# Kernel tuning notes

Measured on AMD Instinct MI355X. Metric: run time of the kernel, lower is better.

The kernel has to match this reference:

```python
import jax, jax.numpy as jnp
import numpy as np

B, L, D, H = 1024, 128, 768, 256
EPS = 1e-5  # torch BatchNorm1d default eps


def _masked_mean(x, lens):
    # x: [B, L, D], lens: [B] int -> mean over first lens[i] rows per sample
    mask = (jnp.arange(x.shape[1])[None, :] < lens[:, None]).astype(x.dtype)  # [B, L]
    return jnp.einsum('bld,bl->bd', x, mask) / lens[:, None].astype(x.dtype)


def _batchnorm_train(x, gamma, beta):
    # training-mode BN: batch mean and biased variance
    mu = jnp.mean(x, axis=0)
    var = jnp.mean((x - mu) ** 2, axis=0)
    return gamma * (x - mu) / jnp.sqrt(var + EPS) + beta


def setup_inputs() -> dict:
    key = jax.random.key(0)
    ks = jax.random.split(key, 12)
    user_features = jax.random.normal(ks[0], (B, L, D), jnp.float32)
    hashtag_features = jax.random.normal(ks[1], (B, L, D), jnp.float32)
    user_lens = jax.random.randint(ks[2], (B,), 1, L + 1, jnp.int32)
    hashtag_lens = jax.random.randint(ks[3], (B,), 1, L + 1, jnp.int32)
    def lin(k, fan_out, fan_in):
        bound = 1.0 / np.sqrt(fan_in)
        kw, kb = jax.random.split(k)
        w = jax.random.uniform(kw, (fan_out, fan_in), jnp.float32, -bound, bound)
        b = jax.random.uniform(kb, (fan_out,), jnp.float32, -bound, bound)
        return w, b
    fc1_w, fc1_b = lin(ks[4], D, 2 * D)
    fc2_w, fc2_b = lin(ks[5], H, D)
    fc3_w, fc3_b = lin(ks[6], 1, H)
    bn1_g = jnp.ones((D,), jnp.float32)
    bn1_b = jnp.zeros((D,), jnp.float32)
    bn2_g = jnp.ones((H,), jnp.float32)
    bn2_b = jnp.zeros((H,), jnp.float32)
    return {
        'user_features': user_features, 'hashtag_features': hashtag_features,
        'user_lens': user_lens, 'hashtag_lens': hashtag_lens,
        'fc1_w': fc1_w, 'fc1_b': fc1_b, 'bn1_g': bn1_g, 'bn1_b': bn1_b,
        'fc2_w': fc2_w, 'fc2_b': fc2_b, 'bn2_g': bn2_g, 'bn2_b': bn2_b,
        'fc3_w': fc3_w, 'fc3_b': fc3_b,
    }


def reference(user_features, hashtag_features, user_lens, hashtag_lens,
              fc1_w, fc1_b, bn1_g, bn1_b, fc2_w, fc2_b, bn2_g, bn2_b,
              fc3_w, fc3_b):
    # fused ragged mean pooling (replaces per-sample python loop)
    u = _masked_mean(user_features, user_lens)       # [B, D]
    h = _masked_mean(hashtag_features, hashtag_lens)  # [B, D]
    x = jnp.concatenate([u, h], axis=1)               # [B, 2D]
    x = jax.nn.relu(_batchnorm_train(x @ fc1_w.T + fc1_b, bn1_g, bn1_b))
    x = jax.nn.relu(_batchnorm_train(x @ fc2_w.T + fc2_b, bn2_g, bn2_b))
    out = jax.nn.sigmoid(x @ fc3_w.T + fc3_b)          # [B, 1]
    return out
```

## Files before the change

kernel.cpp:

```cpp
#include <hip/hip_runtime.h>
#include <cstdint>
#include <cstddef>

#define BATCH 1024
#define SEQL  128
#define DIM   768
#define HID   256
#define KIN1  1536
#define BN_EPS 1e-5f

typedef unsigned short u16;
typedef __attribute__((ext_vector_type(8))) short short8;
typedef __attribute__((ext_vector_type(4))) float f32x4;

__device__ __forceinline__ u16 f2bf(float f) {
  uint32_t u = __float_as_uint(f);
  return (u16)((u + 0x7fffu + ((u >> 16) & 1u)) >> 16);
}
__device__ __forceinline__ f32x4 ntl(const f32x4* p) { return __builtin_nontemporal_load(p); }
__device__ __forceinline__ float kred(float v) {
  v += __shfl_xor(v, 16);
  v += __shfl_xor(v, 32);
  return v;
}

#define POOL_BLK 2048
#define PREP_BLK 168
#define NW1Q (DIM * KIN1 / 4)
#define NWQ  (NW1Q + HID * DIM / 4)

__global__ __launch_bounds__(256) void pool_prep_kernel(
    const float* __restrict__ uf, const float* __restrict__ hf,
    const int* __restrict__ ul, const int* __restrict__ hl,
    const float* __restrict__ w1, const float* __restrict__ w2,
    u16* __restrict__ xb, u16* __restrict__ w1b, u16* __restrict__ w2b) {
  const int id = blockIdx.x;
  const int tid = threadIdx.x;
  if (id < POOL_BLK) {
    __shared__ f32x4 sacc[4][192];
    const int b = id >> 1;
    const int which = id & 1;
    const f32x4* src = (const f32x4*)((which ? hf : uf) + (size_t)b * (SEQL * DIM));
    const int len = which ? hl[b] : ul[b];
    const int wave = tid >> 6, lane = tid & 63;
    f32x4 a0 = (f32x4){0.f, 0.f, 0.f, 0.f}, a1 = a0, a2 = a0;
    f32x4 b0 = a0, b1 = a0, b2 = a0;
    int l = wave;
    for (; l + 4 < len; l += 8) {
      f32x4 v0 = ntl(src + (size_t)l * 192 + lane);
      f32x4 v1 = ntl(src + (size_t)l * 192 + 64 + lane);
      f32x4 v2 = ntl(src + (size_t)l * 192 + 128 + lane);
      f32x4 u0 = ntl(src + (size_t)(l + 4) * 192 + lane);
      f32x4 u1 = ntl(src + (size_t)(l + 4) * 192 + 64 + lane);
      f32x4 u2 = ntl(src + (size_t)(l + 4) * 192 + 128 + lane);
      a0 += v0; a1 += v1; a2 += v2;
      b0 += u0; b1 += u1; b2 += u2;
    }
    if (l < len) {
      a0 += ntl(src + (size_t)l * 192 + lane);
      a1 += ntl(src + (size_t)l * 192 + 64 + lane);
      a2 += ntl(src + (size_t)l * 192 + 128 + lane);
    }
    a0 += b0; a1 += b1; a2 += b2;
    sacc[wave][lane] = a0;
    sacc[wave][64 + lane] = a1;
    sacc[wave][128 + lane] = a2;
    __syncthreads();
    if (tid < 192) {
      f32x4 t = sacc[0][tid] + sacc[1][tid] + sacc[2][tid] + sacc[3][tid];
      const float s = 1.f / (float)len;
      ushort4 o = make_ushort4(f2bf(t[0] * s), f2bf(t[1] * s), f2bf(t[2] * s), f2bf(t[3] * s));
      *(ushort4*)(xb + (size_t)b * KIN1 + which * DIM + tid * 4) = o;
    }
  } else {
    const int j = id - POOL_BLK;
    const int base = j * 256 + tid;
#pragma unroll
    for (int s = 0; s < 8; ++s) {
      const int i = base + s * (PREP_BLK * 256);
      if (i < NW1Q) {
        f32x4 v = ((const f32x4*)w1)[i];
        ((ushort4*)w1b)[i] = make_ushort4(f2bf(v[0]), f2bf(v[1]), f2bf(v[2]), f2bf(v[3]));
      } else {
        const int i2 = i - NW1Q;
        if (i2 < HID * DIM / 4) {
          f32x4 v = ((const f32x4*)w2)[i2];
          ((ushort4*)w2b)[i2] = make_ushort4(f2bf(v[0]), f2bf(v[1]), f2bf(v[2]), f2bf(v[3]));
        }
      }
    }
  }
}

#define LDT 72

__global__ __launch_bounds__(256) void gemm1_kernel(
    const u16* __restrict__ A, const u16* __restrict__ W,
    const float* __restrict__ bias, float* __restrict__ y, float* __restrict__ p1) {
  __shared__ u16 lA[2][64 * LDT];
  __shared__ u16 lB[2][64 * LDT];
  __shared__ float red[2][64][2];
  const int K = KIN1, N = DIM;
  const int tid = threadIdx.x, lane = tid & 63, wv = tid >> 6;
  const int wr = wv >> 1, wc = wv & 1;
  const int r16 = lane & 15, kgrp = lane >> 4;
  const int d = blockIdx.x;
  const int g = d & 7, j = d >> 3;
  const int bm = (g >> 1) * 4 + (j & 3);
  const int bn = (g & 1) * 6 + (j >> 2);
  const int sr = tid >> 3, sc8 = (tid & 7) * 8;

  f32x4 acc[2][2];
#pragma unroll
  for (int mi = 0; mi < 2; ++mi)
#pragma unroll
    for (int ni = 0; ni < 2; ++ni) acc[mi][ni] = (f32x4){0.f, 0.f, 0.f, 0.f};

  const u16* Ab = A + (size_t)bm * 64 * K;
  const u16* Wb = W + (size_t)bn * 64 * K;

  uint4 ra0, ra1, rb0, rb1;
#define G1_LOAD(k0)                                              \
  ra0 = *(const uint4*)(Ab + (size_t)sr * K + (k0) + sc8);       \
  ra1 = *(const uint4*)(Ab + (size_t)(sr + 32) * K + (k0) + sc8);\
  rb0 = *(const uint4*)(Wb + (size_t)sr * K + (k0) + sc8);       \
  rb1 = *(const uint4*)(Wb + (size_t)(sr + 32) * K + (k0) + sc8);
#define G1_WRITE(buf)                                \
  *(uint4*)(lA[buf] + sr * LDT + sc8) = ra0;         \
  *(uint4*)(lA[buf] + (sr + 32) * LDT + sc8) = ra1;  \
  *(uint4*)(lB[buf] + sr * LDT + sc8) = rb0;         \
  *(uint4*)(lB[buf] + (sr + 32) * LDT + sc8) = rb1;

  G1_LOAD(0)
  G1_WRITE(0)
  __syncthreads();
  const int nk = K / 64;
  for (int ti = 0; ti < nk; ++ti) {
    const int cur = ti & 1;
    const bool more = (ti + 1 < nk);
    if (more) { G1_LOAD((ti + 1) * 64) }
#pragma unroll
    for (int kk = 0; kk < 2; ++kk) {
      const int koff = (kk * 4 + kgrp) * 8;
      short8 af0 = *(const short8*)(lA[cur] + (wr * 32 + r16) * LDT + koff);
      short8 af1 = *(const short8*)(lA[cur] + (wr * 32 + 16 + r16) * LDT + koff);
      short8 bf0 = *(const short8*)(lB[cur] + (wc * 32 + r16) * LDT + koff);
      short8 bf1 = *(const short8*)(lB[cur] + (wc * 32 + 16 + r16) * LDT + koff);
      acc[0][0] = __builtin_amdgcn_mfma_f32_16x16x32_bf16(af0, bf0, acc[0][0], 0, 0, 0);
      acc[0][1] = __builtin_amdgcn_mfma_f32_16x16x32_bf16(af0, bf1, acc[0][1], 0, 0, 0);
      acc[1][0] = __builtin_amdgcn_mfma_f32_16x16x32_bf16(af1, bf0, acc[1][0], 0, 0, 0);
      acc[1][1] = __builtin_amdgcn_mfma_f32_16x16x32_bf16(af1, bf1, acc[1][1], 0, 0, 0);
    }
    if (more) { G1_WRITE(cur ^ 1) }
    __syncthreads();
  }
#undef G1_LOAD
#undef G1_WRITE

#pragma unroll
  for (int ni = 0; ni < 2; ++ni) {
    const int col = bn * 64 + wc * 32 + ni * 16 + r16;
    const float bv = bias[col];
    float s = 0.f, s2 = 0.f;
#pragma unroll
    for (int mi = 0; mi < 2; ++mi)
#pragma unroll
      for (int rg = 0; rg < 4; ++rg) {
        const int row = bm * 64 + wr * 32 + mi * 16 + kgrp * 4 + rg;
        const float v = acc[mi][ni][rg] + bv;
        y[(size_t)row * N + col] = v;
        s += v; s2 += v * v;
      }
    s = kred(s); s2 = kred(s2);
    if (lane < 16) {
      red[wr][wc * 32 + ni * 16 + r16][0] = s;
      red[wr][wc * 32 + ni * 16 + r16][1] = s2;
    }
  }
  __syncthreads();
  if (tid < 128) {
    const int col = tid >> 1, wh = tid & 1;
    p1[((size_t)bm * DIM + bn * 64 + col) * 2 + wh] = red[0][col][wh] + red[1][col][wh];
  }
}

__global__ __launch_bounds__(256) void gemm2_kernel(
    const float* __restrict__ y1, const u16* __restrict__ W,
    const float* __restrict__ bias, const float* __restrict__ g, const float* __restrict__ be,
    const float* __restrict__ p1, float* __restrict__ y2, float* __restrict__ p2) {
  __shared__ u16 lA[2][32 * LDT];
  __shared__ u16 lB[2][32 * LDT];
  __shared__ float sS[DIM], sH[DIM];
  __shared__ float red[2][32][2];
  const int K = DIM, N = HID;
  const int tid = threadIdx.x, lane = tid & 63, wv = tid >> 6;
  const int wr = wv >> 1, wc = wv & 1;
  const int r16 = lane & 15, kgrp = lane >> 4;
  const int d = blockIdx.x;
  const int g8 = d & 7, j = d >> 3;
  const int bm = g8 * 4 + (j & 3);
  const int bn = j >> 2;
  const int sr = tid >> 3, sc8 = (tid & 7) * 8;

  for (int c = tid; c < DIM; c += 256) {
    float s = 0.f, s2 = 0.f;
#pragma unroll
    for (int i = 0; i < 16; ++i) {
      float2 pv = *(const float2*)(p1 + ((size_t)i * DIM + c) * 2);
      s += pv.x; s2 += pv.y;
    }
    const float m = s * (1.f / BATCH);
    const float var = s2 * (1.f / BATCH) - m * m;
    const float r = rsqrtf(var + BN_EPS);
    const float scl = r * g[c];
    sS[c] = scl;
    sH[c] = be[c] - m * scl;
  }
  __syncthreads();

  f32x4 acc = (f32x4){0.f, 0.f, 0.f, 0.f};
  const float* Ab = y1 + (size_t)bm * 32 * K;
  const u16* Wb = W + (size_t)bn * 32 * K;

  f32x4 va0, va1;
  uint4 rbq;
#define G2_LOAD(k0)                                          \
  va0 = *(const f32x4*)(Ab + (size_t)sr * K + (k0) + sc8);   \
  va1 = *(const f32x4*)(Ab + (size_t)sr * K + (k0) + sc8 + 4);\
  rbq = *(const uint4*)(Wb + (size_t)sr * K + (k0) + sc8);

  auto pack_write = [&](int buf, int k0) {
    union { ushort us[8]; uint4 q; } pk;
#pragma unroll
    for (int jj = 0; jj < 4; ++jj) {
      pk.us[jj]     = f2bf(fmaxf(0.f, va0[jj] * sS[k0 + sc8 + jj] + sH[k0 + sc8 + jj]));
      pk.us[4 + jj] = f2bf(fmaxf(0.f, va1[jj] * sS[k0 + sc8 + 4 + jj] + sH[k0 + sc8 + 4 + jj]));
    }
    *(uint4*)(lA[buf] + sr * LDT + sc8) = pk.q;
    *(uint4*)(lB[buf] + sr * LDT + sc8) = rbq;
  };

  G2_LOAD(0)
  pack_write(0, 0);
  __syncthreads();
  const int nk = K / 64;
  for (int ti = 0; ti < nk; ++ti) {
    const int cur = ti & 1;
    const bool more = (ti + 1 < nk);
    if (more) { G2_LOAD((ti + 1) * 64) }
#pragma unroll
    for (int kk = 0; kk < 2; ++kk) {
      const int koff = (kk * 4 + kgrp) * 8;
      short8 af0 = *(const short8*)(lA[cur] + (wr * 16 + r16) * LDT + koff);
      short8 bf0 = *(const short8*)(lB[cur] + (wc * 16 + r16) * LDT + koff);
      acc = __builtin_amdgcn_mfma_f32_16x16x32_bf16(af0, bf0, acc, 0, 0, 0);
    }
    if (more) pack_write(cur ^ 1, (ti + 1) * 64);
    __syncthreads();
  }
#undef G2_LOAD

  {
    const int col = bn * 32 + wc * 16 + r16;
    const float bv = bias[col];
    float s = 0.f, s2 = 0.f;
#pragma unroll
    for (int rg = 0; rg < 4; ++rg) {
      const int row = bm * 32 + wr * 16 + kgrp * 4 + rg;
      const float v = acc[rg] + bv;
      y2[(size_t)row * N + col] = v;
      s += v; s2 += v * v;
    }
    s = kred(s); s2 = kred(s2);
    if (lane < 16) {
      red[wr][wc * 16 + r16][0] = s;
      red[wr][wc * 16 + r16][1] = s2;
    }
  }
  __syncthreads();
  if (tid < 64) {
    const int col = tid >> 1, wh = tid & 1;
    p2[((size_t)bm * HID + bn * 32 + col) * 2 + wh] = red[0][col][wh] + red[1][col][wh];
  }
}

__global__ __launch_bounds__(256) void fc3_kernel(
    const float* __restrict__ y2, const float* __restrict__ p2,
    const float* __restrict__ g, const float* __restrict__ be,
    const float* __restrict__ w3, const float* __restrict__ b3, float* __restrict__ out) {
  __shared__ float sS[HID], sH[HID];
  const int tid = threadIdx.x;
  {
    const int c = tid;
    float s = 0.f, s2 = 0.f;
#pragma unroll
    for (int i = 0; i < 32; ++i) {
      float2 pv = *(const float2*)(p2 + ((size_t)i * HID + c) * 2);
      s += pv.x; s2 += pv.y;
    }
    const float m = s * (1.f / BATCH);
    const float var = s2 * (1.f / BATCH) - m * m;
    const float r = rsqrtf(var + BN_EPS);
    const float scl = r * g[c];
    sS[c] = scl;
    sH[c] = be[c] - m * scl;
  }
  __syncthreads();
  const int row = blockIdx.x * 4 + (tid >> 6);
  const int lane = tid & 63;
  f32x4 xv = *(const f32x4*)(y2 + (size_t)row * HID + lane * 4);
  f32x4 sc = *(const f32x4*)&sS[lane * 4];
  f32x4 sh = *(const f32x4*)&sH[lane * 4];
  f32x4 wv = *(const f32x4*)(w3 + lane * 4);
  float dsum = 0.f;
#pragma unroll
  for (int jj = 0; jj < 4; ++jj) dsum += fmaxf(0.f, xv[jj] * sc[jj] + sh[jj]) * wv[jj];
#pragma unroll
  for (int off = 32; off > 0; off >>= 1) dsum += __shfl_xor(dsum, off);
  if (lane == 0) out[row] = 1.f / (1.f + expf(-(dsum + b3[0])));
}

extern "C" void kernel_launch(void* const* d_in, const int* in_sizes, int n_in,
                              void* d_out, int out_size, void* d_ws, size_t ws_size,
                              hipStream_t stream) {
  const float* uf   = (const float*)d_in[0];
  const float* hf   = (const float*)d_in[1];
  const int*   ul   = (const int*)d_in[2];
  const int*   hl   = (const int*)d_in[3];
  const float* fc1w = (const float*)d_in[4];
  const float* fc1b = (const float*)d_in[5];
  const float* bn1g = (const float*)d_in[6];
  const float* bn1b = (const float*)d_in[7];
  const float* fc2w = (const float*)d_in[8];
  const float* fc2b = (const float*)d_in[9];
  const float* bn2g = (const float*)d_in[10];
  const float* bn2b = (const float*)d_in[11];
  const float* fc3w = (const float*)d_in[12];
  const float* fc3b = (const float*)d_in[13];
  float* out = (float*)d_out;

  char* ws = (char*)d_ws;
  u16*   xb  = (u16*)  (ws + 0);
  u16*   w1b = (u16*)  (ws + 3145728);
  u16*   w2b = (u16*)  (ws + 5505024);
  float* y1  = (float*)(ws + 5898240);
  float* y2  = (float*)(ws + 9043968);
  float* p1  = (float*)(ws + 10092544);
  float* p2  = (float*)(ws + 10190848);

  pool_prep_kernel<<<POOL_BLK + PREP_BLK, 256, 0, stream>>>(uf, hf, ul, hl, fc1w, fc2w, xb, w1b, w2b);
  gemm1_kernel<<<192, 256, 0, stream>>>(xb, w1b, fc1b, y1, p1);
  gemm2_kernel<<<256, 256, 0, stream>>>(y1, w2b, fc2b, bn1g, bn1b, p1, y2, p2);
  fc3_kernel<<<256, 256, 0, stream>>>(y2, p2, bn2g, bn2b, fc3w, fc3b, out);
}
```

Measured before the change: 110.4 us.

## Use persistent blocks with atomic ticket scheduling for pooling and weight conversion

Replaces the fixed grid of pooling blocks plus weight-conversion blocks with 1024 persistent blocks that pull jobs from a global atomic ticket counter. Weight-conversion jobs come first in larger chunks, then per-sample pooling jobs. This dynamically balances the ragged per-sample pooling work and cuts block-launch overhead. In exchange it adds a memset launch, an atomic plus two barriers per job, and a dependency on the ticket counter in workspace.

```diff
diff --git a/kernel.cpp b/kernel.cpp
--- a/kernel.cpp
+++ b/kernel.cpp
@@ -24,69 +24,78 @@
   return v;
 }
 
-#define POOL_BLK 2048
-#define PREP_BLK 168
+#define PREP_JOBS 32
+#define PREP_CHUNK 10752
+#define NJOBS (PREP_JOBS + 2048)
 #define NW1Q (DIM * KIN1 / 4)
-#define NWQ  (NW1Q + HID * DIM / 4)
+#define NW2Q (HID * DIM / 4)
 
 __global__ __launch_bounds__(256) void pool_prep_kernel(
     const float* __restrict__ uf, const float* __restrict__ hf,
     const int* __restrict__ ul, const int* __restrict__ hl,
     const float* __restrict__ w1, const float* __restrict__ w2,
-    u16* __restrict__ xb, u16* __restrict__ w1b, u16* __restrict__ w2b) {
-  const int id = blockIdx.x;
+    u16* __restrict__ xb, u16* __restrict__ w1b, u16* __restrict__ w2b,
+    unsigned* __restrict__ ticket) {
+  __shared__ f32x4 sacc[4][192];
+  __shared__ int sjob;
   const int tid = threadIdx.x;
-  if (id < POOL_BLK) {
-    __shared__ f32x4 sacc[4][192];
-    const int b = id >> 1;
-    const int which = id & 1;
-    const f32x4* src = (const f32x4*)((which ? hf : uf) + (size_t)b * (SEQL * DIM));
-    const int len = which ? hl[b] : ul[b];
-    const int wave = tid >> 6, lane = tid & 63;
-    f32x4 a0 = (f32x4){0.f, 0.f, 0.f, 0.f}, a1 = a0, a2 = a0;
-    f32x4 b0 = a0, b1 = a0, b2 = a0;
-    int l = wave;
-    for (; l + 4 < len; l += 8) {
-      f32x4 v0 = ntl(src + (size_t)l * 192 + lane);
-      f32x4 v1 = ntl(src + (size_t)l * 192 + 64 + lane);
-      f32x4 v2 = ntl(src + (size_t)l * 192 + 128 + lane);
-      f32x4 u0 = ntl(src + (size_t)(l + 4) * 192 + lane);
-      f32x4 u1 = ntl(src + (size_t)(l + 4) * 192 + 64 + lane);
-      f32x4 u2 = ntl(src + (size_t)(l + 4) * 192 + 128 + lane);
-      a0 += v0; a1 += v1; a2 += v2;
-      b0 += u0; b1 += u1; b2 += u2;
-    }
-    if (l < len) {
-      a0 += ntl(src + (size_t)l * 192 + lane);
-      a1 += ntl(src + (size_t)l * 192 + 64 + lane);
-      a2 += ntl(src + (size_t)l * 192 + 128 + lane);
-    }
-    a0 += b0; a1 += b1; a2 += b2;
-    sacc[wave][lane] = a0;
-    sacc[wave][64 + lane] = a1;
-    sacc[wave][128 + lane] = a2;
+  const int wave = tid >> 6, lane = tid & 63;
+  for (;;) {
     __syncthreads();
-    if (tid < 192) {
-      f32x4 t = sacc[0][tid] + sacc[1][tid] + sacc[2][tid] + sacc[3][tid];
-      const float s = 1.f / (float)len;
-      ushort4 o = make_ushort4(f2bf(t[0] * s), f2bf(t[1] * s), f2bf(t[2] * s), f2bf(t[3] * s));
-      *(ushort4*)(xb + (size_t)b * KIN1 + which * DIM + tid * 4) = o;
-    }
-  } else {
-    const int j = id - POOL_BLK;
-    const int base = j * 256 + tid;
-#pragma unroll
-    for (int s = 0; s < 8; ++s) {
-      const int i = base + s * (PREP_BLK * 256);
-      if (i < NW1Q) {
-        f32x4 v = ((const f32x4*)w1)[i];
-        ((ushort4*)w1b)[i] = make_ushort4(f2bf(v[0]), f2bf(v[1]), f2bf(v[2]), f2bf(v[3]));
-      } else {
-        const int i2 = i - NW1Q;
-        if (i2 < HID * DIM / 4) {
-          f32x4 v = ((const f32x4*)w2)[i2];
-          ((ushort4*)w2b)[i2] = make_ushort4(f2bf(v[0]), f2bf(v[1]), f2bf(v[2]), f2bf(v[3]));
+    if (tid == 0) sjob = (int)atomicAdd(ticket, 1u);
+    __syncthreads();
+    const int job = sjob;
+    if (job >= NJOBS) return;
+    if (job < PREP_JOBS) {
+      const int base = job * PREP_CHUNK + tid;
+#pragma unroll 2
+      for (int s = 0; s < PREP_CHUNK / 256; ++s) {
+        const int i = base + s * 256;
+        if (i < NW1Q) {
+          f32x4 v = ((const f32x4*)w1)[i];
+          ((ushort4*)w1b)[i] = make_ushort4(f2bf(v[0]), f2bf(v[1]), f2bf(v[2]), f2bf(v[3]));
+        } else {
+          const int i2 = i - NW1Q;
+          if (i2 < NW2Q) {
+            f32x4 v = ((const f32x4*)w2)[i2];
+            ((ushort4*)w2b)[i2] = make_ushort4(f2bf(v[0]), f2bf(v[1]), f2bf(v[2]), f2bf(v[3]));
+          }
         }
+      }
+    } else {
+      const int pj = job - PREP_JOBS;
+      const int b = pj >> 1;
+      const int which = pj & 1;
+      const f32x4* src = (const f32x4*)((which ? hf : uf) + (size_t)b * (SEQL * DIM));
+      const int len = which ? hl[b] : ul[b];
+      f32x4 a0 = (f32x4){0.f, 0.f, 0.f, 0.f}, a1 = a0, a2 = a0;
+      f32x4 b0 = a0, b1 = a0, b2 = a0;
+      int l = wave;
+      for (; l + 4 < len; l += 8) {
+        f32x4 v0 = ntl(src + (size_t)l * 192 + lane);
+        f32x4 v1 = ntl(src + (size_t)l * 192 + 64 + lane);
+        f32x4 v2 = ntl(src + (size_t)l * 192 + 128 + lane);
+        f32x4 u0 = ntl(src + (size_t)(l + 4) * 192 + lane);
+        f32x4 u1 = ntl(src + (size_t)(l + 4) * 192 + 64 + lane);
+        f32x4 u2 = ntl(src + (size_t)(l + 4) * 192 + 128 + lane);
+        a0 += v0; a1 += v1; a2 += v2;
+        b0 += u0; b1 += u1; b2 += u2;
+      }
+      if (l < len) {
+        a0 += ntl(src + (size_t)l * 192 + lane);
+        a1 += ntl(src + (size_t)l * 192 + 64 + lane);
+        a2 += ntl(src + (size_t)l * 192 + 128 + lane);
+      }
+      a0 += b0; a1 += b1; a2 += b2;
+      sacc[wave][lane] = a0;
+      sacc[wave][64 + lane] = a1;
+      sacc[wave][128 + lane] = a2;
+      __syncthreads();
+      if (tid < 192) {
+        f32x4 t = sacc[0][tid] + sacc[1][tid] + sacc[2][tid] + sacc[3][tid];
+        const float s = 1.f / (float)len;
+        ushort4 o = make_ushort4(f2bf(t[0] * s), f2bf(t[1] * s), f2bf(t[2] * s), f2bf(t[3] * s));
+        *(ushort4*)(xb + (size_t)b * KIN1 + which * DIM + tid * 4) = o;
       }
     }
   }
@@ -347,8 +356,10 @@
   float* y2  = (float*)(ws + 9043968);
   float* p1  = (float*)(ws + 10092544);
   float* p2  = (float*)(ws + 10190848);
-
-  pool_prep_kernel<<<POOL_BLK + PREP_BLK, 256, 0, stream>>>(uf, hf, ul, hl, fc1w, fc2w, xb, w1b, w2b);
+  unsigned* ticket = (unsigned*)(ws + 10256384);
+
+  hipMemsetAsync(ticket, 0, 4, stream);
+  pool_prep_kernel<<<1024, 256, 0, stream>>>(uf, hf, ul, hl, fc1w, fc2w, xb, w1b, w2b, ticket);
   gemm1_kernel<<<192, 256, 0, stream>>>(xb, w1b, fc1b, y1, p1);
   gemm2_kernel<<<256, 256, 0, stream>>>(y1, w2b, fc2b, bn1g, bn1b, p1, y2, p2);
   fc3_kernel<<<256, 256, 0, stream>>>(y2, p2, bn2g, bn2b, fc3w, fc3b, out);
```

After: 125.7 us. 13.9% more time.
